# Performance work log

Measured on AMD Instinct MI355X. Metric: run time of the kernel, lower is better.

## Reference

```python
import jax, jax.numpy as jnp
import numpy as np

D_MODEL = 1024
N_HEADS = 16
FEAT_DIM = 16   # q/k head dim before feature-map expansion
V_DIM = 64      # v head dim = d_model / n_heads
EPS = 1e-12


def taylor_exp(x):
    """2nd-order Taylor approx feature map of exp(q^T k / sqrt(d)).
    x: (b, h, l, d) -> (b, h, l, 1 + d + d^2)
    f(x) = [1, x / d^{1/4}, vec(x x^T) / (sqrt(2) * sqrt(d))]
    """
    d = x.shape[-1]
    rd = jnp.sqrt(jnp.float32(d))          # sqrt(d)
    rrd = jnp.sqrt(rd)                     # d^{1/4}
    r2 = jnp.sqrt(jnp.float32(2.0))
    x2 = (x[..., :, None] * x[..., None, :]).reshape(*x.shape[:-1], d * d) / r2
    ones = jnp.ones(x.shape[:-1] + (1,), dtype=x.dtype)
    return jnp.concatenate([ones, x / rrd, x2 / rd], axis=-1)


def setup_inputs() -> dict:
    key = jax.random.key(0)
    k0, k1, k2, k3, k4 = jax.random.split(key, 5)
    b, l = 2, 2048
    scale = 1.0 / np.sqrt(D_MODEL)
    return {
        "hidden_states": jax.random.normal(k0, (b, l, D_MODEL), dtype=jnp.float32),
        "Wq": jax.random.normal(k1, (D_MODEL, N_HEADS * FEAT_DIM), dtype=jnp.float32) * scale,
        "Wk": jax.random.normal(k2, (D_MODEL, N_HEADS * FEAT_DIM), dtype=jnp.float32) * scale,
        "Wv": jax.random.normal(k3, (D_MODEL, N_HEADS * V_DIM), dtype=jnp.float32) * scale,
        "Wo": jax.random.normal(k4, (N_HEADS * V_DIM, D_MODEL), dtype=jnp.float32) * scale,
    }


def reference(hidden_states, Wq, Wk, Wv, Wo):
    b, l, _ = hidden_states.shape
    # projections -> (b, h, l, d)
    q = (hidden_states @ Wq).reshape(b, l, N_HEADS, FEAT_DIM).transpose(0, 2, 1, 3)
    k = (hidden_states @ Wk).reshape(b, l, N_HEADS, FEAT_DIM).transpose(0, 2, 1, 3)
    v = (hidden_states @ Wv).reshape(b, l, N_HEADS, V_DIM).transpose(0, 2, 1, 3)

    qf = taylor_exp(q)  # (b, h, l, 273)
    kf = taylor_exp(k)

    # causal linear attention (naive parallel form used by the torch module)
    A = jnp.einsum('bhnf,bhmf->bhnm', qf, kf)
    A = jnp.tril(A)
    y = jnp.einsum('bhnm,bhme->bhne', A, v)
    # denominator: q_f . cumsum(k_f)
    z = 1.0 / (jnp.einsum('bhlf,bhlf->bhl', qf, jnp.cumsum(kf, axis=2)) + EPS)
    y = y * z[..., None]

    out = y.transpose(0, 2, 1, 3).reshape(b, l, N_HEADS * V_DIM) @ Wo
    return out
```

## Files before the change

kernel.cpp:

```cpp
#include <hip/hip_runtime.h>
#include <hip/hip_bf16.h>

#define BATCH 2
#define LSEQ 2048
#define DMODEL 1024
#define NH 16
#define DQK 16
#define DV 64
#define FDIM 273
#define CHUNK 128
#define NCH (LSEQ / CHUNK)
#define ROWS (BATCH * LSEQ)
#define NBH (BATCH * NH)
#define NBC (NBH * NCH)
#define QKVW 1536
#define C2 0.17677669529663687f

typedef short bf16x8 __attribute__((ext_vector_type(8)));
typedef float f32x4 __attribute__((ext_vector_type(4)));

__device__ __forceinline__ unsigned short f2bf(float f) {
  __hip_bfloat16 h = __float2bfloat16(f);
  unsigned short u; __builtin_memcpy(&u, &h, 2); return u;
}
__device__ __forceinline__ float bf2f(unsigned short u) {
  unsigned int v = (unsigned int)u << 16; float f; __builtin_memcpy(&f, &v, 4); return f;
}

__device__ __forceinline__ void storeC(float* C, size_t off, float v) { C[off] = v; }
__device__ __forceinline__ void storeC(unsigned short* C, size_t off, float v) {
  C[off] = f2bf(v);
}

__global__ __launch_bounds__(256) void prep(
    const float* __restrict__ hs,
    const float* __restrict__ Wq, const float* __restrict__ Wk,
    const float* __restrict__ Wv, const float* __restrict__ Wo,
    unsigned short* __restrict__ hsb,
    unsigned short* __restrict__ wqt, unsigned short* __restrict__ wkt,
    unsigned short* __restrict__ wvt, unsigned short* __restrict__ wot) {
  __shared__ float t[32][33];
  if (blockIdx.z == 4) {
    int bid = blockIdx.y * 32 + blockIdx.x;
    const float4* in4 = (const float4*)hs;
#pragma unroll
    for (int k = 0; k < 4; k++) {
      int i = bid * 1024 + k * 256 + threadIdx.x;
      float4 v = in4[i];
      ushort4 o = {f2bf(v.x), f2bf(v.y), f2bf(v.z), f2bf(v.w)};
      ((ushort4*)hsb)[i] = o;
    }
    return;
  }
  const float* W; unsigned short* Wt; int N;
  switch (blockIdx.z) {
    case 0: W = Wq; Wt = wqt; N = 256; break;
    case 1: W = Wk; Wt = wkt; N = 256; break;
    case 2: W = Wv; Wt = wvt; N = 1024; break;
    default: W = Wo; Wt = wot; N = 1024; break;
  }
  const int nb = blockIdx.x * 32;
  if (nb >= N) return;
  const int kb = blockIdx.y * 32;
  const int tx = threadIdx.x & 31, ty4 = (threadIdx.x >> 5) * 4;
#pragma unroll
  for (int r = 0; r < 4; r++)
    t[ty4 + r][tx] = W[(size_t)(kb + ty4 + r) * N + nb + tx];
  __syncthreads();
#pragma unroll
  for (int r = 0; r < 4; r++)
    Wt[(size_t)(nb + ty4 + r) * DMODEL + kb + tx] = f2bf(t[tx][ty4 + r]);
}

template <typename CT>
__global__ __launch_bounds__(256) void gemm_pipe(
    const unsigned short* __restrict__ A, const unsigned short* __restrict__ Bt,
    CT* __restrict__ C, int M, int N, int K) {
  __shared__ unsigned short Sbuf[4 * 8192];
  const int tid = threadIdx.x;
  const int bm = blockIdx.y * 128, bn = blockIdx.x * 128;
  const int lane = tid & 63;
  const int w = tid >> 6;
  const int qr = (w >> 1) * 64, qc = (w & 1) * 64;
  const int nk = K >> 5;
  f32x4 acc[4][4] = {};

  auto stage = [&](int t) {
    const int k0 = t << 5;
    unsigned short* Sb = Sbuf + (size_t)(t & 3) * 8192;
#pragma unroll
    for (int j = 0; j < 4; ++j) {
      int c = j * 256 + tid;
      int isB = c >> 9;
      int cc = c & 511;
      int row = ((cc >> 6) << 4) + (cc & 15);
      int kh = (cc >> 4) & 3;
      const unsigned short* gp =
          (isB ? Bt + (size_t)(bn + row) * K : A + (size_t)(bm + row) * K) + k0 + kh * 8;
      unsigned short* lp = Sb + isB * 4096 + cc * 8;
      __builtin_amdgcn_global_load_lds(
          (const __attribute__((address_space(1))) unsigned int*)(const void*)gp,
          (__attribute__((address_space(3))) unsigned int*)lp, 16, 0, 0);
    }
  };

#pragma unroll
  for (int t = 0; t < 3; ++t)
    if (t < nk) stage(t);

  for (int t = 0; t < nk; ++t) {
    if (t + 3 < nk) stage(t + 3);
    if      (t + 3 < nk) asm volatile("s_waitcnt vmcnt(12)" ::: "memory");
    else if (t + 2 < nk) asm volatile("s_waitcnt vmcnt(8)" ::: "memory");
    else if (t + 1 < nk) asm volatile("s_waitcnt vmcnt(4)" ::: "memory");
    else                 asm volatile("s_waitcnt vmcnt(0)" ::: "memory");
    __builtin_amdgcn_s_barrier();

    const unsigned short* Ab = Sbuf + (size_t)(t & 3) * 8192;
    const unsigned short* Bb = Ab + 4096;
    bf16x8 a[4], b[4];
#pragma unroll
    for (int i = 0; i < 4; ++i)
      a[i] = *(const bf16x8*)(Ab + ((qr >> 4) + i) * 512 + lane * 8);
#pragma unroll
    for (int i = 0; i < 4; ++i)
      b[i] = *(const bf16x8*)(Bb + ((qc >> 4) + i) * 512 + lane * 8);
#pragma unroll
    for (int i = 0; i < 4; ++i)
#pragma unroll
      for (int jj = 0; jj < 4; ++jj)
        acc[i][jj] = __builtin_amdgcn_mfma_f32_16x16x32_bf16(a[i], b[jj], acc[i][jj], 0, 0, 0);

    __builtin_amdgcn_s_barrier();
    asm volatile("" ::: "memory");
  }

  const int cn = lane & 15, r0 = (lane >> 4) * 4;
#pragma unroll
  for (int i = 0; i < 4; ++i)
#pragma unroll
    for (int jj = 0; jj < 4; ++jj) {
      size_t base = (size_t)(bm + qr + i * 16 + r0) * N + bn + qc + jj * 16 + cn;
#pragma unroll
      for (int r = 0; r < 4; ++r) storeC(C, base + (size_t)r * N, acc[i][jj][r]);
    }
}

__device__ __forceinline__ void stage_Vp(const unsigned short* __restrict__ qkvb,
                                         int row0, int h, int tid, short* Vp) {
#pragma unroll
  for (int it = 0; it < 4; it++) {
    int t = it * 256 + tid;
    int j = t >> 3, e0 = (t & 7) * 8;
    bf16x8 v8 = *(const bf16x8*)(qkvb + (size_t)(row0 + j) * QKVW + 512 + h * 64 + e0);
    int jg = j >> 3, jj = j & 7;
#pragma unroll
    for (int u = 0; u < 8; u++) {
      int e = e0 + u;
      Vp[((e >> 4) * 4 + (jg >> 2)) * 512 + ((jg & 3) * 16 + (e & 15)) * 8 + jj] =
          v8[u];
    }
  }
  {
    int n = tid & 15, jgrp = tid >> 4;
    bf16x8 v8;
#pragma unroll
    for (int u = 0; u < 8; u++) v8[u] = (n == 0) ? (short)0x3F80 : (short)0;
    *(bf16x8*)(Vp + (16 + (jgrp >> 2)) * 512 + ((jgrp & 3) * 16 + n) * 8) = v8;
  }
}

__global__ __launch_bounds__(256) void chunk_sums_mfma(
    const unsigned short* __restrict__ qkvb, unsigned short* __restrict__ Sfrag) {
  const int c = blockIdx.x, bh = blockIdx.y;
  const int b = bh >> 4, h = bh & 15;
  const int tid = threadIdx.x;
  const int lane = tid & 63, w = tid >> 6;
  const int row0 = b * LSEQ + c * CHUNK;

  __shared__ float ksT[16 * 132];
  __shared__ short SH[56 * 512];
  short* Vp = SH;
  short* Kf0 = SH + 20 * 512;
  short* Kf1 = SH + 38 * 512;

  {
    int i = tid >> 1, d0 = (tid & 1) * 8;
    bf16x8 k8 = *(const bf16x8*)(qkvb + (size_t)(row0 + i) * QKVW + 256 + h * 16 + d0);
#pragma unroll
    for (int j = 0; j < 8; j++) ksT[(d0 + j) * 132 + i] = bf2f((unsigned short)k8[j]);
  }
  stage_Vp(qkvb, row0, h, tid, Vp);
  __syncthreads();

  auto gen = [&](int kt, short* dst) {
    for (int o = tid; o < 1152; o += 256) {
      int mt = o >> 6, w6 = o & 63;
      int kh = w6 >> 4, m = w6 & 15;
      int f = mt * 16 + m;
      int i0 = kt * 32 + kh * 8;
      bf16x8 v8;
      if (f == 0) {
#pragma unroll
        for (int j = 0; j < 8; j++) v8[j] = (short)0x3F80;
      } else if (f < 17) {
        const float* ka = &ksT[(f - 1) * 132 + i0];
        float4 a0 = *(const float4*)ka, a1 = *(const float4*)(ka + 4);
        v8[0] = (short)f2bf(0.5f * a0.x); v8[1] = (short)f2bf(0.5f * a0.y);
        v8[2] = (short)f2bf(0.5f * a0.z); v8[3] = (short)f2bf(0.5f * a0.w);
        v8[4] = (short)f2bf(0.5f * a1.x); v8[5] = (short)f2bf(0.5f * a1.y);
        v8[6] = (short)f2bf(0.5f * a1.z); v8[7] = (short)f2bf(0.5f * a1.w);
      } else if (f < FDIM) {
        int ix = f - 17;
        const float* ka = &ksT[(ix >> 4) * 132 + i0];
        const float* kb2 = &ksT[(ix & 15) * 132 + i0];
        float4 a0 = *(const float4*)ka, a1 = *(const float4*)(ka + 4);
        float4 b0 = *(const float4*)kb2, b1 = *(const float4*)(kb2 + 4);
        v8[0] = (short)f2bf(C2 * a0.x * b0.x); v8[1] = (short)f2bf(C2 * a0.y * b0.y);
        v8[2] = (short)f2bf(C2 * a0.z * b0.z); v8[3] = (short)f2bf(C2 * a0.w * b0.w);
        v8[4] = (short)f2bf(C2 * a1.x * b1.x); v8[5] = (short)f2bf(C2 * a1.y * b1.y);
        v8[6] = (short)f2bf(C2 * a1.z * b1.z); v8[7] = (short)f2bf(C2 * a1.w * b1.w);
      } else {
#pragma unroll
        for (int j = 0; j < 8; j++) v8[j] = 0;
      }
      *(bf16x8*)(dst + mt * 512 + (kh * 16 + m) * 8) = v8;
    }
  };

  gen(0, Kf0);
  __syncthreads();

  f32x4 acc[5][5] = {};
  const int nmt = (w < 2) ? 5 : 4;
  for (int kt = 0; kt < 4; kt++) {
    short* cur = (kt & 1) ? Kf1 : Kf0;
    if (kt < 3) gen(kt + 1, (kt & 1) ? Kf0 : Kf1);
    bf16x8 bv[5];
#pragma unroll
    for (int nt = 0; nt < 5; nt++)
      bv[nt] = *(const bf16x8*)(Vp + (nt * 4 + kt) * 512 + lane * 8);
#pragma unroll
    for (int t2 = 0; t2 < 5; t2++) {
      if (t2 < nmt) {
        int mt = w + t2 * 4;
        bf16x8 av = *(const bf16x8*)(cur + mt * 512 + lane * 8);
#pragma unroll
        for (int nt = 0; nt < 5; nt++)
          acc[t2][nt] = __builtin_amdgcn_mfma_f32_16x16x32_bf16(av, bv[nt], acc[t2][nt], 0, 0, 0);
      }
    }
    __syncthreads();
  }

  const int cl = lane & 15, r0q = (lane >> 4) * 4;
#pragma unroll
  for (int t2 = 0; t2 < 5; t2++) {
    if (t2 < nmt) {
      int mt = w + t2 * 4;
#pragma unroll
      for (int reg = 0; reg < 4; reg++) {
        int f = mt * 16 + r0q + reg;
#pragma unroll
        for (int nt = 0; nt < 5; nt++) {
          int e = nt * 16 + cl;
          SH[((f >> 5) * 5 + nt) * 512 + (((f >> 3) & 3) * 16 + (e & 15)) * 8 + (f & 7)] =
              (short)f2bf(acc[t2][nt][reg]);
        }
      }
    }
  }
  __syncthreads();
  unsigned short* dst = Sfrag + ((size_t)bh * NCH + c) * 45 * 512;
  for (int o = tid; o < 2880; o += 256)
    *(bf16x8*)(dst + o * 8) = *(const bf16x8*)(SH + o * 8);
}

__global__ __launch_bounds__(64) void prefix_scan_frag(
    const unsigned short* __restrict__ Sfrag, unsigned short* __restrict__ PG) {
  const int kt5 = blockIdx.x, bh = blockIdx.y;
  const int lane = threadIdx.x;
  float run[8] = {0.f, 0.f, 0.f, 0.f, 0.f, 0.f, 0.f, 0.f};
  const size_t base = ((size_t)bh * NCH * 45 + kt5) * 512 + lane * 8;
#pragma unroll
  for (int cc = 0; cc < NCH; cc++) {
    size_t a = base + (size_t)cc * 45 * 512;
    bf16x8 s8 = *(const bf16x8*)(Sfrag + a);
    bf16x8 o8;
#pragma unroll
    for (int j = 0; j < 8; j++) {
      o8[j] = (short)f2bf(run[j]);
      run[j] += bf2f((unsigned short)s8[j]);
    }
    *(bf16x8*)(PG + a) = o8;
  }
}

__global__ __launch_bounds__(256) void attn_mfma(
    const unsigned short* __restrict__ qkvb, const unsigned short* __restrict__ PG,
    unsigned short* __restrict__ ybuf) {
  const int c = blockIdx.x, bh = blockIdx.y;
  const int b = bh >> 4, h = bh & 15;
  const int tid = threadIdx.x;
  const int lane = tid & 63, w = tid >> 6;
  const int row0 = b * LSEQ + c * CHUNK;

  __shared__ short U[36864];
  __shared__ float denL[128];
  unsigned short* Uu = (unsigned short*)U;

  const int qrow = (w >> 1) * 64 + lane;
  const int shalf = w & 1;
  bf16x8 qa = *(const bf16x8*)(qkvb + (size_t)(row0 + qrow) * QKVW + h * 16);
  bf16x8 qb = *(const bf16x8*)(qkvb + (size_t)(row0 + qrow) * QKVW + h * 16 + 8);

  for (int t = tid; t < 1024; t += 256) {
    int isK = t >> 9;
    int tt = t & 511;
    int i = tt >> 2, kh = tt & 3;
    bf16x8 v8 = {0, 0, 0, 0, 0, 0, 0, 0};
    if (kh < 2)
      v8 = *(const bf16x8*)(qkvb + (size_t)(row0 + i) * QKVW + isK * 256 + h * 16 + kh * 8);
    *(bf16x8*)(U + isK * 4096 + (i >> 4) * 512 + (kh * 16 + (i & 15)) * 8) = v8;
  }
  __syncthreads();

  {
    bf16x8 aq[2];
#pragma unroll
    for (int mi = 0; mi < 2; mi++)
      aq[mi] = *(const bf16x8*)(U + (w * 2 + mi) * 512 + lane * 8);
    f32x4 S[2][8] = {};
#pragma unroll
    for (int nt = 0; nt < 8; nt++) {
      bf16x8 bk = *(const bf16x8*)(U + 4096 + nt * 512 + lane * 8);
#pragma unroll
      for (int mi = 0; mi < 2; mi++)
        S[mi][nt] = __builtin_amdgcn_mfma_f32_16x16x32_bf16(aq[mi], bk, S[mi][nt], 0, 0, 0);
    }
    const int cl = lane & 15, r0q = (lane >> 4) * 4;
#pragma unroll
    for (int mi = 0; mi < 2; mi++)
#pragma unroll
      for (int nt = 0; nt < 8; nt++)
#pragma unroll
        for (int reg = 0; reg < 4; reg++) {
          int i = (w * 2 + mi) * 16 + r0q + reg;
          int j = nt * 16 + cl;
          float s = S[mi][nt][reg];
          float aij = (j <= i) ? fmaf(s, fmaf(s, 0.03125f, 0.25f), 1.0f) : 0.0f;
          U[8192 + ((i >> 4) * 4 + (j >> 5)) * 512 +
            (((j >> 3) & 3) * 16 + (i & 15)) * 8 + (j & 7)] = (short)f2bf(aij);
        }
  }
  stage_Vp(qkvb, row0, h, tid, U + 24576);
  __syncthreads();

  f32x4 Y[2][5] = {};
#pragma unroll
  for (int kc = 0; kc < 4; kc++) {
    bf16x8 a2[2];
#pragma unroll
    for (int mi = 0; mi < 2; mi++)
      a2[mi] = *(const bf16x8*)(U + 8192 + ((w * 2 + mi) * 4 + kc) * 512 + lane * 8);
#pragma unroll
    for (int nt = 0; nt < 5; nt++) {
      bf16x8 b2 = *(const bf16x8*)(U + 24576 + (nt * 4 + kc) * 512 + lane * 8);
#pragma unroll
      for (int mi = 0; mi < 2; mi++)
        Y[mi][nt] = __builtin_amdgcn_mfma_f32_16x16x32_bf16(a2[mi], b2, Y[mi][nt], 0, 0, 0);
    }
  }
  __syncthreads();

  {
    float qv[16], cq[16];
#pragma unroll
    for (int j = 0; j < 8; j++) {
      qv[j] = bf2f((unsigned short)qa[j]);
      qv[8 + j] = bf2f((unsigned short)qb[j]);
    }
#pragma unroll
    for (int j = 0; j < 16; j++) cq[j] = C2 * qv[j];
    unsigned short* qbase = Uu + (qrow >> 4) * 512 + (qrow & 15) * 8;
    if (shalf == 0) {
#pragma unroll
      for (int vk = 0; vk < 18; vk++) {
        bf16x8 v8;
#pragma unroll
        for (int j = 0; j < 8; j++) {
          int f = vk * 8 + j;
          float qf;
          if (f == 0) qf = 1.0f;
          else if (f < 17) qf = 0.5f * qv[f - 1];
          else { int ix = f - 17; qf = cq[ix >> 4] * qv[ix & 15]; }
          v8[j] = (short)f2bf(qf);
        }
        *(bf16x8*)(qbase + (vk >> 2) * 4096 + (vk & 3) * 128) = v8;
      }
    } else {
#pragma unroll
      for (int vk = 18; vk < 36; vk++) {
        bf16x8 v8;
#pragma unroll
        for (int j = 0; j < 8; j++) {
          int f = vk * 8 + j;
          float qf;
          if (f < FDIM) { int ix = f - 17; qf = cq[ix >> 4] * qv[ix & 15]; }
          else qf = 0.0f;
          v8[j] = (short)f2bf(qf);
        }
        *(bf16x8*)(qbase + (vk >> 2) * 4096 + (vk & 3) * 128) = v8;
      }
    }
  }
  __syncthreads();

  const unsigned short* pgl = PG + ((size_t)bh * NCH + c) * 45 * 512 + lane * 8;
#pragma unroll
  for (int ft = 0; ft < 9; ft++) {
    bf16x8 b3[5];
#pragma unroll
    for (int nt = 0; nt < 5; nt++)
      b3[nt] = *(const bf16x8*)(pgl + (ft * 5 + nt) * 512);
    bf16x8 a3[2];
#pragma unroll
    for (int mi = 0; mi < 2; mi++)
      a3[mi] = *(const bf16x8*)(U + ft * 4096 + (w * 2 + mi) * 512 + lane * 8);
#pragma unroll
    for (int nt = 0; nt < 5; nt++)
#pragma unroll
      for (int mi = 0; mi < 2; mi++)
        Y[mi][nt] = __builtin_amdgcn_mfma_f32_16x16x32_bf16(a3[mi], b3[nt], Y[mi][nt], 0, 0, 0);
  }

  const int cl = lane & 15, r0q = (lane >> 4) * 4;
  if (cl == 0) {
#pragma unroll
    for (int mi = 0; mi < 2; mi++)
#pragma unroll
      for (int reg = 0; reg < 4; reg++)
        denL[(w * 2 + mi) * 16 + r0q + reg] = Y[mi][4][reg];
  }
  __syncthreads();
#pragma unroll
  for (int mi = 0; mi < 2; mi++) {
    float invd[4];
#pragma unroll
    for (int reg = 0; reg < 4; reg++)
      invd[reg] = 1.0f / (denL[(w * 2 + mi) * 16 + r0q + reg] + 1e-12f);
#pragma unroll
    for (int nt = 0; nt < 4; nt++)
#pragma unroll
      for (int reg = 0; reg < 4; reg++) {
        int i = (w * 2 + mi) * 16 + r0q + reg;
        int e = nt * 16 + cl;
        ybuf[(size_t)(row0 + i) * (NH * DV) + h * DV + e] =
            f2bf(Y[mi][nt][reg] * invd[reg]);
      }
  }
}

extern "C" void kernel_launch(void* const* d_in, const int* in_sizes, int n_in,
                              void* d_out, int out_size, void* d_ws, size_t ws_size,
                              hipStream_t stream) {
  const float* hs = (const float*)d_in[0];
  const float* Wq = (const float*)d_in[1];
  const float* Wk = (const float*)d_in[2];
  const float* Wv = (const float*)d_in[3];
  const float* Wo = (const float*)d_in[4];
  float* out = (float*)d_out;

  unsigned short* qkvb  = (unsigned short*)d_ws;
  unsigned short* Sfrag = qkvb + (size_t)ROWS * QKVW;
  unsigned short* PG    = Sfrag + (size_t)NBC * 45 * 512;
  unsigned short* hsb   = PG + (size_t)NBC * 45 * 512;
  unsigned short* yb    = hsb;
  unsigned short* wqt   = hsb + (size_t)ROWS * DMODEL;
  unsigned short* wkt   = wqt + (size_t)(NH * DQK) * DMODEL;
  unsigned short* wvt   = wkt + (size_t)(NH * DQK) * DMODEL;
  unsigned short* wot   = wvt + (size_t)(NH * DV) * DMODEL;

  prep<<<dim3(32, 32, 5), 256, 0, stream>>>(hs, Wq, Wk, Wv, Wo, hsb, wqt, wkt, wvt, wot);

  gemm_pipe<unsigned short><<<dim3(QKVW / 128, ROWS / 128), 256, 0, stream>>>(
      hsb, wqt, qkvb, ROWS, QKVW, DMODEL);

  chunk_sums_mfma<<<dim3(NCH, NBH), 256, 0, stream>>>(qkvb, Sfrag);
  prefix_scan_frag<<<dim3(45, NBH), 64, 0, stream>>>(Sfrag, PG);
  attn_mfma<<<dim3(NCH, NBH), 256, 0, stream>>>(qkvb, PG, yb);

  gemm_pipe<float><<<dim3(DMODEL / 128, ROWS / 128), 256, 0, stream>>>(
      yb, wot, out, ROWS, DMODEL, DMODEL);
}
```

Baseline: 168.3 us.

## Process two K-tiles per barrier in GEMM with XCD-aware block remapping

Restructures the bf16 GEMM main loop so each iteration consumes two 32-wide K tiles between barriers, which halves the barrier count, and issues the refill loads after the compute. Block IDs are remapped so consecutive IDs group onto the same XCD for L2 reuse. Global and LDS load addresses are precomputed once, and s_setprio raises wave priority around the MFMA burst. The two-tile loop assumes nk is even and at least three, and the barrier and wait logic with four buffers is delicate.

Measured after the change: 167.8 us. Within noise of the previous version (-0.3%).

```diff
diff --git a/kernel.cpp b/kernel.cpp
--- a/kernel.cpp
+++ b/kernel.cpp
@@ -78,61 +78,76 @@
     CT* __restrict__ C, int M, int N, int K) {
   __shared__ unsigned short Sbuf[4 * 8192];
   const int tid = threadIdx.x;
-  const int bm = blockIdx.y * 128, bn = blockIdx.x * 128;
+  const int nwg = gridDim.x * gridDim.y;
+  const int bid0 = blockIdx.y * gridDim.x + blockIdx.x;
+  const int bid = (bid0 & 7) * (nwg >> 3) + (bid0 >> 3);
+  const int bm = (bid / gridDim.x) * 128, bn = (bid % gridDim.x) * 128;
   const int lane = tid & 63;
   const int w = tid >> 6;
   const int qr = (w >> 1) * 64, qc = (w & 1) * 64;
   const int nk = K >> 5;
   f32x4 acc[4][4] = {};
 
+  const unsigned short* gbase[4];
+  int loff[4];
+#pragma unroll
+  for (int j = 0; j < 4; ++j) {
+    int c = j * 256 + tid;
+    int isB = c >> 9;
+    int cc = c & 511;
+    int row = ((cc >> 6) << 4) + (cc & 15);
+    int kh = (cc >> 4) & 3;
+    gbase[j] = (isB ? Bt + (size_t)(bn + row) * K : A + (size_t)(bm + row) * K) + kh * 8;
+    loff[j] = isB * 4096 + cc * 8;
+  }
   auto stage = [&](int t) {
-    const int k0 = t << 5;
     unsigned short* Sb = Sbuf + (size_t)(t & 3) * 8192;
 #pragma unroll
-    for (int j = 0; j < 4; ++j) {
-      int c = j * 256 + tid;
-      int isB = c >> 9;
-      int cc = c & 511;
-      int row = ((cc >> 6) << 4) + (cc & 15);
-      int kh = (cc >> 4) & 3;
-      const unsigned short* gp =
-          (isB ? Bt + (size_t)(bn + row) * K : A + (size_t)(bm + row) * K) + k0 + kh * 8;
-      unsigned short* lp = Sb + isB * 4096 + cc * 8;
+    for (int j = 0; j < 4; ++j)
       __builtin_amdgcn_global_load_lds(
-          (const __attribute__((address_space(1))) unsigned int*)(const void*)gp,
-          (__attribute__((address_space(3))) unsigned int*)lp, 16, 0, 0);
-    }
+          (const __attribute__((address_space(1))) unsigned int*)(const void*)(gbase[j] + (t << 5)),
+          (__attribute__((address_space(3))) unsigned int*)(Sb + loff[j]), 16, 0, 0);
   };
 
-#pragma unroll
-  for (int t = 0; t < 3; ++t)
-    if (t < nk) stage(t);
-
-  for (int t = 0; t < nk; ++t) {
-    if (t + 3 < nk) stage(t + 3);
-    if      (t + 3 < nk) asm volatile("s_waitcnt vmcnt(12)" ::: "memory");
-    else if (t + 2 < nk) asm volatile("s_waitcnt vmcnt(8)" ::: "memory");
-    else if (t + 1 < nk) asm volatile("s_waitcnt vmcnt(4)" ::: "memory");
-    else                 asm volatile("s_waitcnt vmcnt(0)" ::: "memory");
-    __builtin_amdgcn_s_barrier();
-
-    const unsigned short* Ab = Sbuf + (size_t)(t & 3) * 8192;
-    const unsigned short* Bb = Ab + 4096;
-    bf16x8 a[4], b[4];
-#pragma unroll
-    for (int i = 0; i < 4; ++i)
-      a[i] = *(const bf16x8*)(Ab + ((qr >> 4) + i) * 512 + lane * 8);
-#pragma unroll
-    for (int i = 0; i < 4; ++i)
-      b[i] = *(const bf16x8*)(Bb + ((qc >> 4) + i) * 512 + lane * 8);
-#pragma unroll
-    for (int i = 0; i < 4; ++i)
-#pragma unroll
-      for (int jj = 0; jj < 4; ++jj)
-        acc[i][jj] = __builtin_amdgcn_mfma_f32_16x16x32_bf16(a[i], b[jj], acc[i][jj], 0, 0, 0);
-
+  stage(0); stage(1); stage(2);
+
+  for (int tt = 0; tt < nk; tt += 2) {
+    if (tt + 3 < nk) {
+      stage(tt + 3);
+      asm volatile("s_waitcnt vmcnt(8)" ::: "memory");
+    } else {
+      asm volatile("s_waitcnt vmcnt(0)" ::: "memory");
+    }
     __builtin_amdgcn_s_barrier();
     asm volatile("" ::: "memory");
+
+    const unsigned short* Ab0 = Sbuf + (size_t)(tt & 3) * 8192;
+    const unsigned short* Ab1 = Sbuf + (size_t)((tt + 1) & 3) * 8192;
+    bf16x8 a0[4], b0[4], a1[4], b1[4];
+#pragma unroll
+    for (int i = 0; i < 4; ++i) {
+      a0[i] = *(const bf16x8*)(Ab0 + ((qr >> 4) + i) * 512 + lane * 8);
+      b0[i] = *(const bf16x8*)(Ab0 + 4096 + ((qc >> 4) + i) * 512 + lane * 8);
+      a1[i] = *(const bf16x8*)(Ab1 + ((qr >> 4) + i) * 512 + lane * 8);
+      b1[i] = *(const bf16x8*)(Ab1 + 4096 + ((qc >> 4) + i) * 512 + lane * 8);
+    }
+    __builtin_amdgcn_s_setprio(1);
+#pragma unroll
+    for (int i = 0; i < 4; ++i)
+#pragma unroll
+      for (int jj = 0; jj < 4; ++jj)
+        acc[i][jj] = __builtin_amdgcn_mfma_f32_16x16x32_bf16(a0[i], b0[jj], acc[i][jj], 0, 0, 0);
+#pragma unroll
+    for (int i = 0; i < 4; ++i)
+#pragma unroll
+      for (int jj = 0; jj < 4; ++jj)
+        acc[i][jj] = __builtin_amdgcn_mfma_f32_16x16x32_bf16(a1[i], b1[jj], acc[i][jj], 0, 0, 0);
+    __builtin_amdgcn_s_setprio(0);
+
+    asm volatile("" ::: "memory");
+    __builtin_amdgcn_s_barrier();
+    asm volatile("" ::: "memory");
+    if (tt + 4 < nk) stage(tt + 4);
   }
 
   const int cn = lane & 15, r0 = (lane >> 4) * 4;
```
